# Kernel tuning notes

Measured on AMD Instinct MI355X. Metric: run time of the kernel, lower is better.

## Reference

```python
import jax, jax.numpy as jnp
import numpy as np

IN_C, OUT_C, K, G, STRIDE = 16, 16, 3, 64, 1
B, H, W = 16, 512, 512


def setup_inputs() -> dict:
    key = jax.random.key(0)
    k1, k2, k3 = jax.random.split(key, 3)
    x = jax.random.normal(k1, (B, IN_C, H, W), dtype=jnp.float32)
    spectral_params = jax.random.normal(k2, (K * IN_C, K * OUT_C), dtype=jnp.float32)
    attn_w = jax.random.normal(k3, (G, IN_C), dtype=jnp.float32) * 0.1  # 1x1 conv weight
    attn_b = jnp.zeros((G,), dtype=jnp.float32)                          # 1x1 conv bias
    return {"x": x, "spectral_params": spectral_params, "attn_w": attn_w, "attn_b": attn_b}


def _group_map():
    # radial frequency index over the [K*IN_C, K*OUT_C] spectral grid
    gi = jnp.linspace(-0.5, 0.5, K * IN_C)
    gj = jnp.linspace(-0.5, 0.5, K * OUT_C)
    idx = jnp.sqrt(gi[:, None] ** 2 + gj[None, :] ** 2)
    thresholds = jnp.linspace(0.0, 0.5, G + 1)
    # bucket i satisfies thresholds[i] <= idx < thresholds[i+1]
    gid = jnp.searchsorted(thresholds, idx, side='right') - 1
    valid = (idx < 0.5) & (gid >= 0) & (gid < G)
    return jnp.where(valid, gid, 0), valid


def reference(x, spectral_params, attn_w, attn_b):
    b, c, h, w = x.shape
    gid, valid = _group_map()  # [KC, KO] int, [KC, KO] bool
    # attention gate: global avg pool -> 1x1 conv -> sigmoid  -> [b, G]
    pooled = x.mean(axis=(2, 3))                              # [b, c]
    pi = jax.nn.sigmoid(pooled @ attn_w.T + attn_b)           # [b, G]
    # group masks are disjoint radial bands, so the mixture collapses to a
    # per-element gather of the gate value (0 outside all bands)
    gate = jnp.where(valid[None], pi[:, gid], 0.0)            # [b, KC, KO]
    dyn = spectral_params[None] * gate                        # [b, KC, KO]
    # view(in, k, out, k).permute(2,0,1,3) -> [b, out, in, k, k]
    dyn = dyn.reshape(b, IN_C, K, OUT_C, K).transpose(0, 3, 1, 2, 4)
    kernel = dyn.reshape(b * OUT_C, IN_C, K, K)
    # per-sample dynamic conv as a single grouped conv (groups = batch)
    out = jax.lax.conv_general_dilated(
        x.reshape(1, b * c, h, w), kernel,
        window_strides=(STRIDE, STRIDE), padding='VALID',
        dimension_numbers=('NCHW', 'OIHW', 'NCHW'),
        feature_group_count=b)
    return out.reshape(b, OUT_C, out.shape[2], out.shape[3])
```

## Files before the change

### kernel.cpp

```cpp
#include <hip/hip_runtime.h>


#define BATCH 16
#define CH 16
#define HIN 512
#define WIN 512
#define HOUT 510
#define WOUT 510

typedef _Float16 half8 __attribute__((ext_vector_type(8)));
typedef float f32x4 __attribute__((ext_vector_type(4)));


__global__ __launch_bounds__(256) void transform_kernel(const float* __restrict__ x,
                                                        unsigned short* __restrict__ xt,
                                                        float* __restrict__ psum) {
    const int blk = blockIdx.x;
    const int b = blk >> 7, within = blk & 127;
    const int tid = threadIdx.x;
    float s[16];
#pragma unroll
    for (int c = 0; c < 16; ++c) s[c] = 0.f;
    const float* xb = x + ((size_t)b << 22);
#pragma unroll
    for (int m = 0; m < 8; ++m) {
        const int p = within * 2048 + m * 256 + tid;
        union { _Float16 h[16]; uint4 q[2]; } u;
#pragma unroll
        for (int c = 0; c < 16; ++c) {
            float v = xb[(c << 18) + p];
            s[c] += v;
            u.h[c] = (_Float16)v;
        }
        uint4* dst = (uint4*)(xt + (((size_t)(b << 18) + p) << 4));
        dst[0] = u.q[0];
        dst[1] = u.q[1];
    }
    const int lane = tid & 63, w = tid >> 6;
#pragma unroll
    for (int c = 0; c < 16; ++c) {
        float r = s[c];
        r += __shfl_xor(r, 1);  r += __shfl_xor(r, 2);  r += __shfl_xor(r, 4);
        r += __shfl_xor(r, 8);  r += __shfl_xor(r, 16); r += __shfl_xor(r, 32);
        s[c] = r;
    }
    if (lane == 0) {
        float* ps = psum + (size_t)(b * 512 + within * 4 + w) * 16;
#pragma unroll
        for (int c = 0; c < 16; ++c) ps[c] = s[c];
    }
}

__global__ __launch_bounds__(256) void stage2_kernel(const float* __restrict__ psum,
                                                     const float* __restrict__ attn_w,
                                                     const float* __restrict__ attn_b,
                                                     const float* __restrict__ spectral,
                                                     unsigned short* __restrict__ wpack) {
    const int b = blockIdx.x, t = threadIdx.x;
    const int c = t & 15, ch = t >> 4;
    float s = 0.f;
    for (int m = 0; m < 32; ++m) s += psum[(size_t)(b * 512 + ch + m * 16) * 16 + c];
    __shared__ float red[256];
    __shared__ float pooled[16];
    __shared__ float pis[64];
    red[t] = s;
    __syncthreads();
    for (int off = 8; off; off >>= 1) {
        if (ch < off) red[t] += red[t + off * 16];
        __syncthreads();
    }
    if (t < 16) pooled[t] = red[t] * (1.f / 262144.f);
    __syncthreads();
    if (t < 64) {
        float a = attn_b[t];
#pragma unroll
        for (int c2 = 0; c2 < 16; ++c2) a += pooled[c2] * attn_w[t * 16 + c2];
        pis[t] = 1.f / (1.f + expf(-a));
    }
    __syncthreads();
    for (int e = t; e < 320; e += 256) {
        const int c5 = e >> 6, lane = e & 63;
        const int o = lane & 15, g = lane >> 4;
        union { _Float16 h[8]; uint4 q; } u;
#pragma unroll
        for (int j = 0; j < 8; ++j) {
            const int kap = c5 * 32 + g * 8 + j;
            const int tp = kap >> 4, i = kap & 15;
            float wv = 0.f;
            if (tp < 9) {
                const int ki = tp / 3, kj = tp - ki * 3;
                const int r = i * 3 + ki, cc = o * 3 + kj;
                const float gi = -0.5f + (float)r * (1.f / 47.f);
                const float gj = -0.5f + (float)cc * (1.f / 47.f);
                const float d2 = gi * gi + gj * gj;
                if (d2 < 0.25f) {
                    int gid = (int)(sqrtf(d2) * 128.f);
                    gid = gid < 63 ? gid : 63;
                    wv = spectral[r * 48 + cc] * pis[gid];
                }
            }
            u.h[j] = (_Float16)wv;
        }
        *(uint4*)(wpack + ((size_t)(b * 5 + c5) * 64 + lane) * 8) = u.q;
    }
}

#define PITCH 4224
__global__ __launch_bounds__(256) void conv_mfma_kernel(const unsigned short* __restrict__ xt,
                                                        const unsigned short* __restrict__ wpack,
                                                        float* __restrict__ out) {
    const int b = blockIdx.y;
    const int cg = blockIdx.x & 3;
    const int yg = blockIdx.x >> 2;
    const int tid = threadIdx.x;
    const int lane = tid & 63, wv = tid >> 6;
    const int y0 = yg * 4, x0g = cg * 128;

    __shared__ unsigned char lds[6 * PITCH];

    half8 wf[5];
    {
        const uint4* wp = (const uint4*)wpack + (size_t)b * 5 * 64 + lane;
#pragma unroll
        for (int c5 = 0; c5 < 5; ++c5) wf[c5] = __builtin_bit_cast(half8, wp[c5 * 64]);
    }

    for (int e = tid; e < 1560; e += 256) {
        const int rr = e / 260;
        const int rem = e - rr * 260;
        const int p = rem >> 1, h = rem & 1;
        int ir = y0 + rr;  ir = ir < 511 ? ir : 511;
        int ic = x0g + p;  ic = ic < 511 ? ic : 511;
        const uint4 v = *(const uint4*)(xt + ((((size_t)b << 18) + (ir << 9) + ic) << 4) + h * 8);
        unsigned a = (unsigned)(rr * PITCH + p * 32 + h * 16);
        a ^= (a >> 3) & 0x30u;
        *(uint4*)(lds + a) = v;
    }
    __syncthreads();

    const int n = lane & 15, g = lane >> 4;
    const int y = y0 + wv;

    unsigned base[5];
#pragma unroll
    for (int c5 = 0; c5 < 5; ++c5) {
        const int tp = 2 * c5 + (g >> 1);
        unsigned a;
        if (tp == 9) {
            a = 0;
        } else {
            const int dy = tp / 3, dx = tp - dy * 3;
            a = (unsigned)((wv + dy) * PITCH + (n + dx) * 32 + (g & 1) * 16);
            a ^= (a >> 3) & 0x30u;
        }
        base[c5] = a;
    }

    const bool ymask = (y < HOUT);
    float* dst0 = out + ((size_t)(b * 16 + n) * HOUT + y) * WOUT + x0g + g * 4;

#pragma unroll
    for (int tt = 0; tt < 8; ++tt) {
        half8 xf[5];
#pragma unroll
        for (int c5 = 0; c5 < 5; ++c5)
            xf[c5] = __builtin_bit_cast(half8, *(const uint4*)(lds + (base[c5] + tt * 512)));
        f32x4 acc = {0.f, 0.f, 0.f, 0.f};
#pragma unroll
        for (int c5 = 0; c5 < 5; ++c5)
            acc = __builtin_amdgcn_mfma_f32_16x16x32_f16(xf[c5], wf[c5], acc, 0, 0, 0);
        if (ymask) {
            const int pb = x0g + tt * 16 + g * 4;
            float* dst = dst0 + tt * 16;
            if (pb + 3 < WOUT) {
                *(float2*)dst = make_float2(acc[0], acc[1]);
                *(float2*)(dst + 2) = make_float2(acc[2], acc[3]);
            } else {
#pragma unroll
                for (int r = 0; r < 4; ++r)
                    if (pb + r < WOUT) dst[r] = acc[r];
            }
        }
    }
}

#define TW 128
#define TH 8
#define XW 132

__global__ __launch_bounds__(256) void pool_kernel(const float* __restrict__ x,
                                                   float* __restrict__ pooled) {
    const int bc = blockIdx.x;
    const float4* src = (const float4*)(x + ((size_t)bc << 18));
    float s = 0.f;
    for (int e = threadIdx.x; e < (HIN * WIN / 4); e += 256) {
        float4 v = src[e];
        s += (v.x + v.y) + (v.z + v.w);
    }
    __shared__ float red[256];
    red[threadIdx.x] = s;
    __syncthreads();
    for (int off = 128; off > 0; off >>= 1) {
        if (threadIdx.x < off) red[threadIdx.x] += red[threadIdx.x + off];
        __syncthreads();
    }
    if (threadIdx.x == 0) pooled[bc] = red[0] * (1.0f / (HIN * WIN));
}

__global__ __launch_bounds__(256) void attn_kernel(const float* __restrict__ pooled,
                                                   const float* __restrict__ attn_w,
                                                   const float* __restrict__ attn_b,
                                                   float* __restrict__ pi) {
    int t = blockIdx.x * 256 + threadIdx.x;
    if (t >= BATCH * 64) return;
    int b = t >> 6, g = t & 63;
    float s = attn_b[g];
#pragma unroll
    for (int c = 0; c < CH; ++c) s += pooled[b * CH + c] * attn_w[g * CH + c];
    pi[t] = 1.0f / (1.0f + expf(-s));
}

__global__ __launch_bounds__(256) void weight_kernel(const float* __restrict__ spectral,
                                                     const float* __restrict__ pi,
                                                     float* __restrict__ wbuf) {
    int idx = blockIdx.x * 256 + threadIdx.x;
    if (idx >= BATCH * CH * CH * 12) return;
    int tap = idx % 12;
    int o = (idx / 12) % CH;
    int i = (idx / 192) % CH;
    int b = idx / 3072;
    float w = 0.f;
    if (tap < 9) {
        int ki = tap / 3, kj = tap % 3;
        int r = i * 3 + ki, c = o * 3 + kj;
        float gi = -0.5f + (float)r * (1.0f / 47.0f);
        float gj = -0.5f + (float)c * (1.0f / 47.0f);
        float d2 = gi * gi + gj * gj;
        if (d2 < 0.25f) {
            int gid = (int)(sqrtf(d2) * 128.0f);
            gid = gid < 63 ? gid : 63;
            w = spectral[r * 48 + c] * pi[b * 64 + gid];
        }
    }
    wbuf[idx] = w;
}

__global__ __launch_bounds__(256) void conv_kernel(const float* __restrict__ x,
                                                   const float* __restrict__ wbuf,
                                                   float* __restrict__ out) {
    const int b = blockIdx.y;
    const int tc = blockIdx.x & 3;
    const int tr = blockIdx.x >> 2;
    __shared__ float xs[10 * XW];
    __shared__ float ws[CH * CH * 12];
    {
        const float4* src = (const float4*)(wbuf + (size_t)b * (CH * CH * 12));
        float4* dst = (float4*)ws;
        for (int e = threadIdx.x; e < 768; e += 256) dst[e] = src[e];
    }
    const int r0 = tr * TH, c0 = tc * TW;
    const int px = (threadIdx.x & 31) * 4, py = threadIdx.x >> 5;
    float acc[16][4];
#pragma unroll
    for (int o = 0; o < 16; ++o)
#pragma unroll
        for (int p = 0; p < 4; ++p) acc[o][p] = 0.f;
    for (int i = 0; i < CH; ++i) {
        __syncthreads();
        const float* xsrc = x + (((size_t)b * CH + i) << 18);
        for (int e = threadIdx.x; e < 330; e += 256) {
            int rr = e / 33;
            int c4 = (e - rr * 33) * 4;
            int ir = r0 + rr, ic = c0 + c4;
            float4 v;
            if (ir < HIN && ic + 3 < WIN) {
                v = *(const float4*)(xsrc + ((size_t)ir << 9) + ic);
            } else {
                v.x = v.y = v.z = v.w = 0.f;
                if (ir < HIN) {
                    const float* row = xsrc + ((size_t)ir << 9);
                    if (ic + 0 < WIN) v.x = row[ic + 0];
                    if (ic + 1 < WIN) v.y = row[ic + 1];
                    if (ic + 2 < WIN) v.z = row[ic + 2];
                    if (ic + 3 < WIN) v.w = row[ic + 3];
                }
            }
            *(float4*)(xs + rr * XW + c4) = v;
        }
        __syncthreads();
        float xv[3][8];
#pragma unroll
        for (int kr = 0; kr < 3; ++kr) {
            float4 a = *(const float4*)(xs + (py + kr) * XW + px);
            float4 c = *(const float4*)(xs + (py + kr) * XW + px + 4);
            xv[kr][0] = a.x; xv[kr][1] = a.y; xv[kr][2] = a.z; xv[kr][3] = a.w;
            xv[kr][4] = c.x; xv[kr][5] = c.y; xv[kr][6] = c.z; xv[kr][7] = c.w;
        }
#pragma unroll
        for (int o = 0; o < 16; ++o) {
            const float* wrow = ws + (i * 16 + o) * 12;
            float4 w0 = *(const float4*)wrow;
            float4 w1 = *(const float4*)(wrow + 4);
            float w8 = wrow[8];
#pragma unroll
            for (int p = 0; p < 4; ++p) {
                float s = acc[o][p];
                s += xv[0][p + 0] * w0.x;
                s += xv[0][p + 1] * w0.y;
                s += xv[0][p + 2] * w0.z;
                s += xv[1][p + 0] * w0.w;
                s += xv[1][p + 1] * w1.x;
                s += xv[1][p + 2] * w1.y;
                s += xv[2][p + 0] * w1.z;
                s += xv[2][p + 1] * w1.w;
                s += xv[2][p + 2] * w8;
                acc[o][p] = s;
            }
        }
    }
    const int oy = r0 + py, ox = c0 + px;
    if (oy < HOUT) {
#pragma unroll
        for (int o = 0; o < 16; ++o) {
            float* orow = out + (((size_t)(b * 16 + o)) * HOUT + oy) * WOUT + ox;
            if (ox + 3 < WOUT) {
                ((float2*)orow)[0] = make_float2(acc[o][0], acc[o][1]);
                ((float2*)orow)[1] = make_float2(acc[o][2], acc[o][3]);
            } else {
#pragma unroll
                for (int p = 0; p < 4; ++p)
                    if (ox + p < WOUT) orow[p] = acc[o][p];
            }
        }
    }
}

extern "C" void kernel_launch(void* const* d_in, const int* in_sizes, int n_in,
                              void* d_out, int out_size, void* d_ws, size_t ws_size,
                              hipStream_t stream) {
    const float* x = (const float*)d_in[0];
    const float* spectral = (const float*)d_in[1];
    const float* attn_w = (const float*)d_in[2];
    const float* attn_b = (const float*)d_in[3];
    float* out = (float*)d_out;

    const size_t XT_BYTES = (size_t)16 * 512 * 512 * 16 * 2;
    const size_t PSUM_BYTES = (size_t)16 * 512 * 16 * 4;
    const size_t WPACK_BYTES = (size_t)16 * 5 * 64 * 8 * 2;
    const size_t NEED = XT_BYTES + PSUM_BYTES + WPACK_BYTES;

    if (ws_size >= NEED) {
        unsigned short* xt = (unsigned short*)d_ws;
        float* psum = (float*)((char*)d_ws + XT_BYTES);
        unsigned short* wpack = (unsigned short*)((char*)d_ws + XT_BYTES + PSUM_BYTES);

        transform_kernel<<<dim3(2048), dim3(256), 0, stream>>>(x, xt, psum);
        stage2_kernel<<<dim3(16), dim3(256), 0, stream>>>(psum, attn_w, attn_b, spectral, wpack);
        conv_mfma_kernel<<<dim3(512, 16), dim3(256), 0, stream>>>(xt, wpack, out);
    } else {
        float* ws = (float*)d_ws;
        float* pooled = ws;
        float* pi = ws + 256;
        float* wbuf = ws + 1280;
        pool_kernel<<<dim3(BATCH * CH), dim3(256), 0, stream>>>(x, pooled);
        attn_kernel<<<dim3(4), dim3(256), 0, stream>>>(pooled, attn_w, attn_b, pi);
        weight_kernel<<<dim3((BATCH * CH * CH * 12 + 255) / 256), dim3(256), 0, stream>>>(spectral, pi, wbuf);
        conv_kernel<<<dim3(4 * 64, BATCH), dim3(256), 0, stream>>>(x, wbuf, out);
    }
}
```

Baseline: 224.3 us.

## Vectorize transform loads, enlarge conv row tile, use nontemporal output stores

The transform kernel now reads four consecutive pixels per channel with 128-bit nontemporal loads and writes eight 16-byte packed fp16 vectors per thread. It uses twice as many blocks, and the partial-sum buffer and stage2 reduction are resized to match. The conv kernel moves to 512 threads covering 8 output rows per block, so the 2-row halo is amortized over more rows at the cost of a larger LDS tile. Output stores become nontemporal, aiming to cut cache pollution from the large streaming result write.

After: 371.6 us. +65.7%, slower.

```diff
diff --git a/kernel.cpp b/kernel.cpp
--- a/kernel.cpp
+++ b/kernel.cpp
@@ -10,33 +10,38 @@
 
 typedef _Float16 half8 __attribute__((ext_vector_type(8)));
 typedef float f32x4 __attribute__((ext_vector_type(4)));
+typedef float f32x2 __attribute__((ext_vector_type(2)));
 
 
 __global__ __launch_bounds__(256) void transform_kernel(const float* __restrict__ x,
                                                         unsigned short* __restrict__ xt,
                                                         float* __restrict__ psum) {
     const int blk = blockIdx.x;
-    const int b = blk >> 7, within = blk & 127;
+    const int b = blk >> 8, within = blk & 255;
     const int tid = threadIdx.x;
+    const int p0 = (within * 256 + tid) * 4;
+    const float* xb = x + ((size_t)b << 22);
+
+    f32x4 v[16];
     float s[16];
 #pragma unroll
-    for (int c = 0; c < 16; ++c) s[c] = 0.f;
-    const float* xb = x + ((size_t)b << 22);
-#pragma unroll
-    for (int m = 0; m < 8; ++m) {
-        const int p = within * 2048 + m * 256 + tid;
-        union { _Float16 h[16]; uint4 q[2]; } u;
-#pragma unroll
-        for (int c = 0; c < 16; ++c) {
-            float v = xb[(c << 18) + p];
-            s[c] += v;
-            u.h[c] = (_Float16)v;
-        }
-        uint4* dst = (uint4*)(xt + (((size_t)(b << 18) + p) << 4));
-        dst[0] = u.q[0];
-        dst[1] = u.q[1];
-    }
-    const int lane = tid & 63, w = tid >> 6;
+    for (int c = 0; c < 16; ++c) {
+        v[c] = __builtin_nontemporal_load((const f32x4*)(xb + ((size_t)c << 18) + p0));
+        s[c] = (v[c][0] + v[c][1]) + (v[c][2] + v[c][3]);
+    }
+
+    union { _Float16 h[64]; uint4 q[8]; } u;
+#pragma unroll
+    for (int c = 0; c < 16; ++c) {
+        u.h[0 * 16 + c] = (_Float16)v[c][0];
+        u.h[1 * 16 + c] = (_Float16)v[c][1];
+        u.h[2 * 16 + c] = (_Float16)v[c][2];
+        u.h[3 * 16 + c] = (_Float16)v[c][3];
+    }
+    uint4* dst = (uint4*)(xt + ((size_t)((b << 18) + p0)) * 16);
+#pragma unroll
+    for (int k = 0; k < 8; ++k) dst[k] = u.q[k];
+
 #pragma unroll
     for (int c = 0; c < 16; ++c) {
         float r = s[c];
@@ -44,8 +49,8 @@
         r += __shfl_xor(r, 8);  r += __shfl_xor(r, 16); r += __shfl_xor(r, 32);
         s[c] = r;
     }
-    if (lane == 0) {
-        float* ps = psum + (size_t)(b * 512 + within * 4 + w) * 16;
+    if ((tid & 63) == 0) {
+        float* ps = psum + (size_t)(b * 1024 + within * 4 + (tid >> 6)) * 16;
 #pragma unroll
         for (int c = 0; c < 16; ++c) ps[c] = s[c];
     }
@@ -57,16 +62,16 @@
                                                      const float* __restrict__ spectral,
                                                      unsigned short* __restrict__ wpack) {
     const int b = blockIdx.x, t = threadIdx.x;
-    const int c = t & 15, ch = t >> 4;
+    const int c = t & 15, m = t >> 4;
     float s = 0.f;
-    for (int m = 0; m < 32; ++m) s += psum[(size_t)(b * 512 + ch + m * 16) * 16 + c];
+    for (int j = 0; j < 64; ++j) s += psum[((size_t)b * 1024 + m + j * 16) * 16 + c];
     __shared__ float red[256];
     __shared__ float pooled[16];
     __shared__ float pis[64];
     red[t] = s;
     __syncthreads();
     for (int off = 8; off; off >>= 1) {
-        if (ch < off) red[t] += red[t + off * 16];
+        if (m < off) red[t] += red[t + off * 16];
         __syncthreads();
     }
     if (t < 16) pooled[t] = red[t] * (1.f / 262144.f);
@@ -106,7 +111,7 @@
 }
 
 #define PITCH 4224
-__global__ __launch_bounds__(256) void conv_mfma_kernel(const unsigned short* __restrict__ xt,
+__global__ __launch_bounds__(512) void conv_mfma_kernel(const unsigned short* __restrict__ xt,
                                                         const unsigned short* __restrict__ wpack,
                                                         float* __restrict__ out) {
     const int b = blockIdx.y;
@@ -114,9 +119,9 @@
     const int yg = blockIdx.x >> 2;
     const int tid = threadIdx.x;
     const int lane = tid & 63, wv = tid >> 6;
-    const int y0 = yg * 4, x0g = cg * 128;
-
-    __shared__ unsigned char lds[6 * PITCH];
+    const int y0 = yg * 8, x0g = cg * 128;
+
+    __shared__ unsigned char lds[10 * PITCH];
 
     half8 wf[5];
     {
@@ -125,7 +130,7 @@
         for (int c5 = 0; c5 < 5; ++c5) wf[c5] = __builtin_bit_cast(half8, wp[c5 * 64]);
     }
 
-    for (int e = tid; e < 1560; e += 256) {
+    for (int e = tid; e < 2600; e += 512) {
         const int rr = e / 260;
         const int rem = e - rr * 260;
         const int p = rem >> 1, h = rem & 1;
@@ -173,8 +178,8 @@
             const int pb = x0g + tt * 16 + g * 4;
             float* dst = dst0 + tt * 16;
             if (pb + 3 < WOUT) {
-                *(float2*)dst = make_float2(acc[0], acc[1]);
-                *(float2*)(dst + 2) = make_float2(acc[2], acc[3]);
+                __builtin_nontemporal_store((f32x2){acc[0], acc[1]}, (f32x2*)dst);
+                __builtin_nontemporal_store((f32x2){acc[2], acc[3]}, (f32x2*)(dst + 2));
             } else {
 #pragma unroll
                 for (int r = 0; r < 4; ++r)
@@ -345,7 +350,7 @@
     float* out = (float*)d_out;
 
     const size_t XT_BYTES = (size_t)16 * 512 * 512 * 16 * 2;
-    const size_t PSUM_BYTES = (size_t)16 * 512 * 16 * 4;
+    const size_t PSUM_BYTES = (size_t)16 * 1024 * 16 * 4;
     const size_t WPACK_BYTES = (size_t)16 * 5 * 64 * 8 * 2;
     const size_t NEED = XT_BYTES + PSUM_BYTES + WPACK_BYTES;
 
@@ -354,9 +359,9 @@
         float* psum = (float*)((char*)d_ws + XT_BYTES);
         unsigned short* wpack = (unsigned short*)((char*)d_ws + XT_BYTES + PSUM_BYTES);
 
-        transform_kernel<<<dim3(2048), dim3(256), 0, stream>>>(x, xt, psum);
+        transform_kernel<<<dim3(4096), dim3(256), 0, stream>>>(x, xt, psum);
         stage2_kernel<<<dim3(16), dim3(256), 0, stream>>>(psum, attn_w, attn_b, spectral, wpack);
-        conv_mfma_kernel<<<dim3(512, 16), dim3(256), 0, stream>>>(xt, wpack, out);
+        conv_mfma_kernel<<<dim3(256, 16), dim3(512), 0, stream>>>(xt, wpack, out);
     } else {
         float* ws = (float*)d_ws;
         float* pooled = ws;
```
